# Kernel tuning notes

Measured on AMD Instinct MI355X. Metric: run time of the kernel, lower is better.

Reference implementation:

```python
import jax, jax.numpy as jnp
import numpy as np

N = 50000      # nodes
E = 1600000    # edges (avg degree 32)
D = 128        # feature dim (hardcoded by GATConv(128,128,1))
K = 3          # propagation order
NEG_SLOPE = 0.2  # DGL GATConv default leaky_relu slope


def setup_inputs() -> dict:
    key = jax.random.key(0)
    k1, k2, k3, k4, k5, k6, k7 = jax.random.split(key, 7)
    feats = jax.random.normal(k1, (N, D), dtype=jnp.float32)
    src = jax.random.randint(k2, (E,), 0, N, dtype=jnp.int32)
    dst = jax.random.randint(k3, (E,), 0, N, dtype=jnp.int32)
    W = jax.random.normal(k4, (D, D), dtype=jnp.float32) * 0.05
    attn_l = jax.random.normal(k5, (D,), dtype=jnp.float32) * 0.05
    attn_r = jax.random.normal(k6, (D,), dtype=jnp.float32) * 0.05
    bias = jax.random.normal(k7, (D,), dtype=jnp.float32) * 0.05
    return {"feats": feats, "W": W, "attn_l": attn_l, "attn_r": attn_r,
            "bias": bias, "src": src, "dst": dst}


def _grand_conv(feats, src, dst, order):
    seg = jax.ops.segment_sum
    ones = jnp.ones((src.shape[0],), feats.dtype)
    deg_in = jnp.maximum(seg(ones, dst, num_segments=N), 1.0)
    deg_out = jnp.maximum(seg(ones, src, num_segments=N), 1.0)
    norm1 = deg_in ** -0.5   # dst-side (in-degree) norm
    norm2 = deg_out ** -0.5  # src-side (out-degree) norm
    # rst = D_in^-1/2 A D_out^-1/2 feats  (one SpMM)
    nf = feats * norm2[:, None]
    rst = seg(nf[src], dst, num_segments=N) * norm1[:, None]
    # edge weight = norm1[src] * norm2[dst]  (fn.u_mul_v)
    w = (norm1[src] * norm2[dst])[:, None]  # [E,1]
    x = rst
    y = feats  # note: rst itself is NOT added (faithful to source)
    for _ in range(order):
        x = seg(x[src] * w, dst, num_segments=N)  # SpMM hop
        y = y + x
    return y / (order + 1)


def _gat(feat, W, attn_l, attn_r, bias, src, dst):
    seg = jax.ops.segment_sum
    h = feat @ W                      # [N,D]
    el = h @ attn_l                   # [N]
    er = h @ attn_r                   # [N]
    e = jax.nn.leaky_relu(el[src] + er[dst], NEG_SLOPE)  # [E]
    m = jax.ops.segment_max(e, dst, num_segments=N)      # stable edge-softmax
    a = jnp.exp(e - m[dst])
    s = seg(a, dst, num_segments=N)
    alpha = a / s[dst]
    out = seg(h[src] * alpha[:, None], dst, num_segments=N)
    return jax.nn.relu(out + bias)


def reference(feats, W, attn_l, attn_r, bias, src, dst):
    # drop_node with rate 0.0 is identity; S=1 so stacked mean is identity too.
    feat = _grand_conv(feats, src, dst, K)
    logits = _gat(feat, W, attn_l, attn_r, bias, src, dst)
    return jax.nn.log_softmax(logits, axis=-1)
```

## Files before the change

kernel.cpp:

```cpp
#include <hip/hip_runtime.h>
#include <hip/hip_bf16.h>
#include <math.h>

#define D 128
#define SB 512
#define GNUM 256
#define MAXW4 12512

typedef __attribute__((ext_vector_type(8))) short bf16x8;
typedef __attribute__((ext_vector_type(4))) float f32x4;
typedef __attribute__((ext_vector_type(2))) float fv2;

__device__ __forceinline__ bf16x8 pack8(const float* r) {
    union { bf16x8 v; __hip_bfloat162 h[4]; } u;
#pragma unroll
    for (int i = 0; i < 4; ++i)
        u.h[i] = __float22bfloat162_rn(make_float2(r[2 * i], r[2 * i + 1]));
    return u.v;
}

__device__ __forceinline__ uint2 packfp8x8(const float* r) {
    unsigned int w0 = 0, w1 = 0;
    w0 = __builtin_amdgcn_cvt_pk_fp8_f32(r[0], r[1], w0, false);
    w0 = __builtin_amdgcn_cvt_pk_fp8_f32(r[2], r[3], w0, true);
    w1 = __builtin_amdgcn_cvt_pk_fp8_f32(r[4], r[5], w1, false);
    w1 = __builtin_amdgcn_cvt_pk_fp8_f32(r[6], r[7], w1, true);
    return make_uint2(w0, w1);
}

__device__ __forceinline__ uint4 packfp8x16(const float* r) {
    uint4 o;
    unsigned int w;
    w = 0;
    w = __builtin_amdgcn_cvt_pk_fp8_f32(r[0], r[1], w, false);
    w = __builtin_amdgcn_cvt_pk_fp8_f32(r[2], r[3], w, true);
    o.x = w;
    w = 0;
    w = __builtin_amdgcn_cvt_pk_fp8_f32(r[4], r[5], w, false);
    w = __builtin_amdgcn_cvt_pk_fp8_f32(r[6], r[7], w, true);
    o.y = w;
    w = 0;
    w = __builtin_amdgcn_cvt_pk_fp8_f32(r[8], r[9], w, false);
    w = __builtin_amdgcn_cvt_pk_fp8_f32(r[10], r[11], w, true);
    o.z = w;
    w = 0;
    w = __builtin_amdgcn_cvt_pk_fp8_f32(r[12], r[13], w, false);
    w = __builtin_amdgcn_cvt_pk_fp8_f32(r[14], r[15], w, true);
    o.w = w;
    return o;
}

__device__ __forceinline__ void acc_fp8x16(uint4 v, fv2* a) {
    a[0] += __builtin_amdgcn_cvt_pk_f32_fp8(v.x, false);
    a[1] += __builtin_amdgcn_cvt_pk_f32_fp8(v.x, true);
    a[2] += __builtin_amdgcn_cvt_pk_f32_fp8(v.y, false);
    a[3] += __builtin_amdgcn_cvt_pk_f32_fp8(v.y, true);
    a[4] += __builtin_amdgcn_cvt_pk_f32_fp8(v.z, false);
    a[5] += __builtin_amdgcn_cvt_pk_f32_fp8(v.z, true);
    a[6] += __builtin_amdgcn_cvt_pk_f32_fp8(v.w, false);
    a[7] += __builtin_amdgcn_cvt_pk_f32_fp8(v.w, true);
}

__device__ __forceinline__ void acc_fp8x16w(uint4 v, float w, fv2* a) {
    fv2 wv = {w, w};
    a[0] += wv * __builtin_amdgcn_cvt_pk_f32_fp8(v.x, false);
    a[1] += wv * __builtin_amdgcn_cvt_pk_f32_fp8(v.x, true);
    a[2] += wv * __builtin_amdgcn_cvt_pk_f32_fp8(v.y, false);
    a[3] += wv * __builtin_amdgcn_cvt_pk_f32_fp8(v.y, true);
    a[4] += wv * __builtin_amdgcn_cvt_pk_f32_fp8(v.z, false);
    a[5] += wv * __builtin_amdgcn_cvt_pk_f32_fp8(v.z, true);
    a[6] += wv * __builtin_amdgcn_cvt_pk_f32_fp8(v.w, false);
    a[7] += wv * __builtin_amdgcn_cvt_pk_f32_fp8(v.w, true);
}

__device__ __forceinline__ float fast_exp2(float x) {
#if __has_builtin(__builtin_amdgcn_exp2f)
    return __builtin_amdgcn_exp2f(x);
#else
    return exp2f(x);
#endif
}

__global__ __launch_bounds__(256) void histo_both(const int* __restrict__ src,
                                                  const int* __restrict__ dst,
                                                  unsigned int* __restrict__ Hs,
                                                  unsigned int* __restrict__ Hd,
                                                  int E, int N) {
    __shared__ unsigned int h[2 * MAXW4];
    int words = (N + 3) >> 2;
    for (int i = threadIdx.x; i < 2 * words; i += 256) h[i] = 0;
    __syncthreads();
    int per = (E + GNUM - 1) / GNUM;
    int lo = blockIdx.x * per;
    int hi = min(E, lo + per);
    for (int e = lo + (int)threadIdx.x; e < hi; e += 256) {
        int s = src[e];
        int d = dst[e];
        atomicAdd(&h[s >> 2], 1u << ((s & 3) * 8));
        atomicAdd(&h[words + (d >> 2)], 1u << ((d & 3) * 8));
    }
    __syncthreads();
    unsigned int* hsrow = Hs + (size_t)blockIdx.x * words;
    unsigned int* hdrow = Hd + (size_t)blockIdx.x * words;
    for (int i = threadIdx.x; i < words; i += 256) {
        hsrow[i] = h[i];
        hdrow[i] = h[words + i];
    }
}

__global__ void col_sum8(const unsigned char* __restrict__ H, float* __restrict__ n2, int N) {
    int bin = blockIdx.x * blockDim.x + threadIdx.x;
    if (bin >= N) return;
    size_t stride = (size_t)(((N + 3) >> 2) * 4);
    unsigned int s = 0;
    for (int b = 0; b < GNUM; ++b) s += H[(size_t)b * stride + bin];
    n2[bin] = rsqrtf((float)max((int)s, 1));
}

__global__ void col_scan8(unsigned char* __restrict__ Hd, int* __restrict__ deg_in,
                          float* __restrict__ n1, int N) {
    int bin = blockIdx.x * blockDim.x + threadIdx.x;
    if (bin >= N) return;
    size_t stride = (size_t)(((N + 3) >> 2) * 4);
    unsigned int run = 0;
    for (int b = 0; b < GNUM; ++b) {
        size_t o = (size_t)b * stride + bin;
        unsigned int hv = Hd[o];
        Hd[o] = (unsigned char)run;
        run += hv;
    }
    deg_in[bin] = (int)run;
    n1[bin] = rsqrtf((float)max((int)run, 1));
}

__global__ void scan_blocks(const int* __restrict__ in, int* __restrict__ out,
                            int* __restrict__ sums, int n) {
    __shared__ int sh[SB];
    int gid = blockIdx.x * SB + threadIdx.x;
    int v = (gid < n) ? in[gid] : 0;
    sh[threadIdx.x] = v;
    __syncthreads();
    for (int off = 1; off < SB; off <<= 1) {
        int t = (threadIdx.x >= off) ? sh[threadIdx.x - off] : 0;
        __syncthreads();
        sh[threadIdx.x] += t;
        __syncthreads();
    }
    if (gid < n) out[gid] = sh[threadIdx.x] - v;
    if (threadIdx.x == SB - 1) sums[blockIdx.x] = sh[threadIdx.x];
}

__global__ void scan_sums(int* sums, int nb) {
    __shared__ int sh[SB];
    int v = (threadIdx.x < nb) ? sums[threadIdx.x] : 0;
    sh[threadIdx.x] = v;
    __syncthreads();
    for (int off = 1; off < SB; off <<= 1) {
        int t = (threadIdx.x >= off) ? sh[threadIdx.x - off] : 0;
        __syncthreads();
        sh[threadIdx.x] += t;
        __syncthreads();
    }
    if (threadIdx.x < nb) sums[threadIdx.x] = sh[threadIdx.x] - v;
}

__global__ void scan_add(int* out, const int* __restrict__ sums, int n, int E) {
    int gid = blockIdx.x * SB + threadIdx.x;
    if (gid < n) out[gid] += sums[blockIdx.x];
    if (blockIdx.x == 0 && threadIdx.x == 0) out[n] = E;
}

__global__ __launch_bounds__(256) void fill_part(const int* __restrict__ src,
                                                 const int* __restrict__ dst,
                                                 const int* __restrict__ rowp,
                                                 const unsigned char* __restrict__ base,
                                                 int* __restrict__ csr, int E, int N) {
    __shared__ unsigned int cur[MAXW4];
    int words = (N + 3) >> 2;
    for (int i = threadIdx.x; i < words; i += 256) cur[i] = 0;
    __syncthreads();
    size_t stride = (size_t)(words * 4);
    int per = (E + GNUM - 1) / GNUM;
    int lo = blockIdx.x * per;
    int hi = min(E, lo + per);
    const unsigned char* brow = base + (size_t)blockIdx.x * stride;
    for (int e = lo + (int)threadIdx.x; e < hi; e += 256) {
        int d = dst[e];
        unsigned int sh = (d & 3) * 8;
        unsigned int r = atomicAdd(&cur[d >> 2], 1u << sh);
        int rank = (int)((r >> sh) & 0xFFu);
        int pos = rowp[d] + (int)brow[d] + rank;
        csr[pos] = src[e];
    }
}

__global__ void convert_nf8(const float* __restrict__ feats, const float* __restrict__ n2,
                            unsigned int* __restrict__ nf8, int N) {
    int t = blockIdx.x * blockDim.x + threadIdx.x;
    int n = t >> 5, l = t & 31;
    if (n >= N) return;
    float w = n2[n];
    float4 f = *reinterpret_cast<const float4*>(feats + (size_t)n * D + l * 4);
    unsigned int w0 = 0;
    w0 = __builtin_amdgcn_cvt_pk_fp8_f32(f.x * w, f.y * w, w0, false);
    w0 = __builtin_amdgcn_cvt_pk_fp8_f32(f.z * w, f.w * w, w0, true);
    nf8[(size_t)n * 32 + l] = w0;
}

__global__ void convert_W(const float* __restrict__ W, ushort* __restrict__ Wb) {
    int tid = blockIdx.x * blockDim.x + threadIdx.x;
    if (tid >= 2048) return;
    int c = tid >> 8, t = (tid >> 6) & 3, lane = tid & 63;
    int col = c * 16 + (lane & 15);
    int k0 = t * 32 + ((lane >> 4) << 3);
    ushort* outp = Wb + (size_t)tid * 8;
    for (int j = 0; j < 8; ++j) {
        __hip_bfloat16 b = __float2bfloat16(W[(size_t)(k0 + j) * D + col]);
        outp[j] = *reinterpret_cast<ushort*>(&b);
    }
}

template <int MODE>
__global__ __launch_bounds__(256) void spmmw(const uint4* __restrict__ xs16,
                                             const ushort* __restrict__ ypin,
                                             const float* __restrict__ feats,
                                             const int* __restrict__ rowp,
                                             const int* __restrict__ csr,
                                             const float* __restrict__ n1,
                                             const float* __restrict__ n2,
                                             ushort* __restrict__ yp,
                                             uint4* __restrict__ outs16, int N) {
    int lane = threadIdx.x & 63;
    int g = lane >> 3, c = lane & 7;
    int wid = ((blockIdx.x * blockDim.x + threadIdx.x) >> 6) * 8 + g;
    if (wid >= N) return;
    int beg = rowp[wid], end = rowp[wid + 1];
    fv2 acc2[8] = {{0.f, 0.f}, {0.f, 0.f}, {0.f, 0.f}, {0.f, 0.f},
                   {0.f, 0.f}, {0.f, 0.f}, {0.f, 0.f}, {0.f, 0.f}};
    int base = beg;
    int cur_s = (beg < end) ? csr[beg + min(c, end - beg - 1)] : 0;
    while (base < end) {
        int nb = base + 8;
        int next_s = 0;
        if (nb < end) next_s = csr[nb + min(c, end - nb - 1)];
        int kn = min(8, end - base);
        uint4 v[8];
#pragma unroll
        for (int k = 0; k < 8; ++k) {
            int sk = __shfl(cur_s, k, 8);
            if (k < kn) v[k] = xs16[(size_t)sk * 8 + c];
        }
#pragma unroll
        for (int k = 0; k < 8; ++k)
            if (k < kn) acc_fp8x16(v[k], acc2);
        cur_s = next_s;
        base = nb;
    }
    float acc[16];
#pragma unroll
    for (int j = 0; j < 8; ++j) {
        acc[2 * j] = acc2[j][0];
        acc[2 * j + 1] = acc2[j][1];
    }
    if (MODE == 0) {
        float s1 = n1[wid];
        float sc = s1 * s1;
        float r[16];
#pragma unroll
        for (int i = 0; i < 16; ++i) r[i] = acc[i] * sc;
        outs16[(size_t)wid * 8 + c] = packfp8x16(r);
    } else if (MODE == 1 || MODE == 2) {
        float sp = n2[wid];
        float ss = sp * n1[wid];
        float xv[16], rs[16];
#pragma unroll
        for (int i = 0; i < 16; ++i) { xv[i] = acc[i] * sp; rs[i] = acc[i] * ss; }
        if (MODE == 2) {
            const bf16x8* pv = reinterpret_cast<const bf16x8*>(ypin + (size_t)wid * 128 + c * 16);
#pragma unroll
            for (int hb = 0; hb < 2; ++hb) {
                bf16x8 prev = pv[hb];
                const __hip_bfloat162* h2 = reinterpret_cast<const __hip_bfloat162*>(&prev);
#pragma unroll
                for (int i = 0; i < 4; ++i) {
                    float2 v2 = __bfloat1622float2(h2[i]);
                    xv[8 * hb + 2 * i] += v2.x;
                    xv[8 * hb + 2 * i + 1] += v2.y;
                }
            }
        }
        bf16x8* ov = reinterpret_cast<bf16x8*>(yp + (size_t)wid * 128 + c * 16);
        ov[0] = pack8(xv);
        ov[1] = pack8(xv + 8);
        outs16[(size_t)wid * 8 + c] = packfp8x16(rs);
    } else {
        float sp = n2[wid];
        float ft[16];
#pragma unroll
        for (int q4 = 0; q4 < 4; ++q4) {
            float4 f = *reinterpret_cast<const float4*>(feats + (size_t)wid * D + c * 16 + q4 * 4);
            ft[4 * q4] = f.x; ft[4 * q4 + 1] = f.y; ft[4 * q4 + 2] = f.z; ft[4 * q4 + 3] = f.w;
        }
        float r[16];
        const bf16x8* pv = reinterpret_cast<const bf16x8*>(ypin + (size_t)wid * 128 + c * 16);
#pragma unroll
        for (int hb = 0; hb < 2; ++hb) {
            bf16x8 prev = pv[hb];
            const __hip_bfloat162* h2 = reinterpret_cast<const __hip_bfloat162*>(&prev);
#pragma unroll
            for (int i = 0; i < 4; ++i) {
                float2 v2 = __bfloat1622float2(h2[i]);
                r[8 * hb + 2 * i]     = 0.25f * (ft[8 * hb + 2 * i] + v2.x + acc[8 * hb + 2 * i] * sp);
                r[8 * hb + 2 * i + 1] = 0.25f * (ft[8 * hb + 2 * i + 1] + v2.y + acc[8 * hb + 2 * i + 1] * sp);
            }
        }
        bf16x8* ov = reinterpret_cast<bf16x8*>(yp + (size_t)wid * 128 + c * 16);
        ov[0] = pack8(r);
        ov[1] = pack8(r + 8);
    }
}

__global__ __launch_bounds__(256) void gatw(const uint4* __restrict__ h16,
                                            const int* __restrict__ rowp,
                                            const int* __restrict__ csr,
                                            const float2* __restrict__ elsc,
                                            const float* __restrict__ er,
                                            const float* __restrict__ bias,
                                            float* __restrict__ out, int N) {
    int lane = threadIdx.x & 63;
    int g = lane >> 3, c = lane & 7;
    int wid = ((blockIdx.x * blockDim.x + threadIdx.x) >> 6) * 8 + g;
    if (wid >= N) return;
    int beg = rowp[wid], end = rowp[wid + 1];
    float ern = er[wid];
    float psum = 0.f;
    fv2 acc2[8] = {{0.f, 0.f}, {0.f, 0.f}, {0.f, 0.f}, {0.f, 0.f},
                   {0.f, 0.f}, {0.f, 0.f}, {0.f, 0.f}, {0.f, 0.f}};
    int base = beg;
    int cur_s = (beg < end) ? csr[beg + min(c, end - beg - 1)] : 0;
    while (base < end) {
        int nb = base + 8;
        int next_s = 0;
        if (nb < end) next_s = csr[nb + min(c, end - nb - 1)];
        int kn = min(8, end - base);
        float2 es = elsc[cur_s];
        float t = es.x + ern;
        t = fmaxf(t, 0.2f * t);
        float p = (c < kn) ? fast_exp2(t) : 0.f;
        psum += p;
        float wv = p * es.y;
        uint4 v[8];
#pragma unroll
        for (int k = 0; k < 8; ++k) {
            int sk = __shfl(cur_s, k, 8);
            if (k < kn) v[k] = h16[(size_t)sk * 8 + c];
        }
#pragma unroll
        for (int k = 0; k < 8; ++k)
            if (k < kn) {
                float wk = __shfl(wv, k, 8);
                acc_fp8x16w(v[k], wk, acc2);
            }
        cur_s = next_s;
        base = nb;
    }
    psum += __shfl_xor(psum, 1, 8);
    psum += __shfl_xor(psum, 2, 8);
    psum += __shfl_xor(psum, 4, 8);
    float inv = psum > 0.f ? 1.f / psum : 0.f;
    float zA[8], zB[8];
    float mx = -INFINITY;
#pragma unroll
    for (int j = 0; j < 8; ++j) {
        float2 b2 = *reinterpret_cast<const float2*>(bias + 16 * j + 2 * c);
        zA[j] = fmaxf(acc2[j >> 1][j & 1] * inv + b2.x, 0.f);
        zB[j] = fmaxf(acc2[(j + 8) >> 1][(j + 8) & 1] * inv + b2.y, 0.f);
        mx = fmaxf(mx, fmaxf(zA[j], zB[j]));
    }
    mx = fmaxf(mx, __shfl_xor(mx, 1, 8));
    mx = fmaxf(mx, __shfl_xor(mx, 2, 8));
    mx = fmaxf(mx, __shfl_xor(mx, 4, 8));
    float pz = 0.f;
#pragma unroll
    for (int j = 0; j < 8; ++j) pz += __expf(zA[j] - mx) + __expf(zB[j] - mx);
    pz += __shfl_xor(pz, 1, 8);
    pz += __shfl_xor(pz, 2, 8);
    pz += __shfl_xor(pz, 4, 8);
    float ls = logf(pz);
    float* op = out + (size_t)wid * D;
#pragma unroll
    for (int j = 0; j < 8; ++j) {
        float2 o2 = make_float2(zA[j] - mx - ls, zB[j] - mx - ls);
        *reinterpret_cast<float2*>(op + 16 * j + 2 * c) = o2;
    }
}

__global__ __launch_bounds__(256) void gemm_mfma(const ushort* __restrict__ ybf,
                                                 const ushort* __restrict__ Wb,
                                                 const float* __restrict__ attnl,
                                                 const float* __restrict__ attnr,
                                                 unsigned char* __restrict__ h8,
                                                 float2* __restrict__ elsc,
                                                 float* __restrict__ er, int N) {
    __shared__ ushort Ws[16384];
    {
        const float4* srcv = reinterpret_cast<const float4*>(Wb);
        float4* dstv = reinterpret_cast<float4*>(Ws);
        for (int i = threadIdx.x; i < 2048; i += 256) dstv[i] = srcv[i];
    }
    __syncthreads();
    int wave = threadIdx.x >> 6, lane = threadIdx.x & 63;
    int base = blockIdx.x * 64 + wave * 16;
    if (base >= N) return;
    int col16 = lane & 15, rgrp = lane >> 4;

    int arow = base + col16;
    const bf16x8* yrow = reinterpret_cast<const bf16x8*>(ybf + (size_t)arow * 128);
    bf16x8 afrag[4];
#pragma unroll
    for (int t = 0; t < 4; ++t) afrag[t] = yrow[t * 4 + rgrp];

    const bf16x8* WsV = reinterpret_cast<const bf16x8*>(Ws);
    f32x4 acc[8];
#pragma unroll
    for (int c = 0; c < 8; ++c) acc[c] = (f32x4){0.f, 0.f, 0.f, 0.f};
#pragma unroll
    for (int c = 0; c < 8; ++c) {
#pragma unroll
        for (int t = 0; t < 4; ++t) {
            bf16x8 b = WsV[(c * 4 + t) * 64 + lane];
            acc[c] = __builtin_amdgcn_mfma_f32_16x16x32_bf16(afrag[t], b, acc[c], 0, 0, 0);
        }
    }

    float pl[4] = {0.f, 0.f, 0.f, 0.f}, pr[4] = {0.f, 0.f, 0.f, 0.f};
#pragma unroll
    for (int c = 0; c < 8; ++c) {
        float alc = attnl[c * 16 + col16];
        float arc = attnr[c * 16 + col16];
#pragma unroll
        for (int r = 0; r < 4; ++r) {
            pl[r] += acc[c][r] * alc;
            pr[r] += acc[c][r] * arc;
        }
    }
#pragma unroll
    for (int r = 0; r < 4; ++r) {
#pragma unroll
        for (int off = 8; off; off >>= 1) {
            pl[r] += __shfl_xor(pl[r], off);
            pr[r] += __shfl_xor(pr[r], off);
        }
    }

    float rmax[4];
#pragma unroll
    for (int r = 0; r < 4; ++r) {
        float m = 0.f;
#pragma unroll
        for (int c = 0; c < 8; ++c) m = fmaxf(m, fabsf(acc[c][r]));
#pragma unroll
        for (int off = 1; off < 16; off <<= 1) m = fmaxf(m, __shfl_xor(m, off));
        rmax[r] = fmaxf(m, 1e-20f);
    }

#pragma unroll
    for (int r = 0; r < 4; ++r) {
        float iv = 448.f / rmax[r];
        float rr[8];
#pragma unroll
        for (int c = 0; c < 8; ++c) rr[c] = acc[c][r] * iv;
        uint2 pk = packfp8x8(rr);
        int row = base + rgrp * 4 + r;
        *reinterpret_cast<uint2*>(h8 + (size_t)row * 128 + col16 * 8) = pk;
    }

    const float LOG2E = 1.44269504088896340736f;
    if (col16 == 0) {
#pragma unroll
        for (int r = 0; r < 4; ++r) {
            int row = base + rgrp * 4 + r;
            elsc[row] = make_float2(pl[r] * LOG2E, rmax[r] * (1.f / 448.f));
            er[row] = pr[r] * LOG2E;
        }
    }
}

extern "C" void kernel_launch(void* const* d_in, const int* in_sizes, int n_in,
                              void* d_out, int out_size, void* d_ws, size_t ws_size,
                              hipStream_t stream) {
    const float* feats  = (const float*)d_in[0];
    const float* W      = (const float*)d_in[1];
    const float* attn_l = (const float*)d_in[2];
    const float* attn_r = (const float*)d_in[3];
    const float* bias   = (const float*)d_in[4];
    const int*   src    = (const int*)d_in[5];
    const int*   dst    = (const int*)d_in[6];
    int N = in_sizes[0] / D;
    int E = in_sizes[5];
    float* out = (float*)d_out;

    char* p = (char*)d_ws;
    auto alloc = [&](size_t bytes) {
        char* r = p;
        p += (bytes + 255) & ~size_t(255);
        return r;
    };
    int*    deg_in = (int*)alloc((size_t)N * 4);
    int*    rowp   = (int*)alloc(((size_t)N + 1) * 4);
    int*    bsums  = (int*)alloc((size_t)SB * 4);
    float*  n1     = (float*)alloc((size_t)N * 4);
    float*  n2     = (float*)alloc((size_t)N * 4);
    float*  er     = (float*)alloc((size_t)N * 4);
    float2* elsc   = (float2*)alloc((size_t)N * 8);
    int*    csr    = (int*)alloc((size_t)E * 4);
    ushort* Wb     = (ushort*)alloc((size_t)16384 * 2);
    ushort* bufY1  = (ushort*)alloc((size_t)N * 128 * 2);
    ushort* bufY   = (ushort*)alloc((size_t)N * 128 * 2);
    uint4*  t0     = (uint4*)alloc((size_t)N * 8 * 16);
    uint4*  t1     = (uint4*)alloc((size_t)N * 8 * 16);
    uint4*  t2     = (uint4*)alloc((size_t)N * 8 * 16);
    unsigned int* Hs = (unsigned int*)bufY1;
    unsigned int* Hd = (unsigned int*)bufY;

    const int tb = 256;
    histo_both<<<GNUM, tb, 0, stream>>>(src, dst, Hs, Hd, E, N);
    col_sum8<<<(N + tb - 1) / tb, tb, 0, stream>>>((const unsigned char*)Hs, n2, N);
    col_scan8<<<(N + tb - 1) / tb, tb, 0, stream>>>((unsigned char*)Hd, deg_in, n1, N);
    int nb = (N + SB - 1) / SB;
    scan_blocks<<<nb, SB, 0, stream>>>(deg_in, rowp, bsums, N);
    scan_sums<<<1, SB, 0, stream>>>(bsums, nb);
    scan_add<<<nb, SB, 0, stream>>>(rowp, bsums, N, E);
    fill_part<<<GNUM, tb, 0, stream>>>(src, dst, rowp, (const unsigned char*)Hd, csr, E, N);
    convert_W<<<8, tb, 0, stream>>>(W, Wb);
    convert_nf8<<<((size_t)N * 32 + tb - 1) / tb, tb, 0, stream>>>(feats, n2,
                                                                   (unsigned int*)t1, N);

    int wgrid8 = (N + 31) / 32;
    spmmw<0><<<wgrid8, 256, 0, stream>>>(t1, nullptr, nullptr, rowp, csr, n1, n2,
                                         nullptr, t0, N);
    spmmw<1><<<wgrid8, 256, 0, stream>>>(t0, nullptr, nullptr, rowp, csr, n1, n2,
                                         bufY1, t1, N);
    spmmw<2><<<wgrid8, 256, 0, stream>>>(t1, bufY1, nullptr, rowp, csr, n1, n2,
                                         bufY1, t2, N);
    spmmw<3><<<wgrid8, 256, 0, stream>>>(t2, bufY1, feats, rowp, csr, n1, n2,
                                         bufY, nullptr, N);

    gemm_mfma<<<(N + 63) / 64, 256, 0, stream>>>(bufY, Wb, attn_l, attn_r,
                                                 (unsigned char*)t0, elsc, er, N);
    gatw<<<wgrid8, 256, 0, stream>>>((const uint4*)t0, rowp, csr, elsc, er, bias, out, N);
}
```

Baseline: 263.2 us.

## Double-buffer neighbor row gathers in SpMM and GAT kernels with full/remainder split

Restructures the per-node neighbor loops in spmmw and gatw so that the next batch of 8 fp8 feature rows is loaded into a second register buffer while the current batch is accumulated. Full groups of 8 edges run without per-element bounds checks, and the partial tail is handled separately. Addresses are computed with 32-bit shift/or instead of size_t multiplies. This aims to hide gather latency, at the cost of doubled vector registers (vA/vB), which may reduce occupancy.

```diff
diff --git a/kernel.cpp b/kernel.cpp
--- a/kernel.cpp
+++ b/kernel.cpp
@@ -235,26 +235,63 @@
     int wid = ((blockIdx.x * blockDim.x + threadIdx.x) >> 6) * 8 + g;
     if (wid >= N) return;
     int beg = rowp[wid], end = rowp[wid + 1];
+    int cnt = end - beg;
+    int nfull = cnt >> 3;
+    int rem = cnt & 7;
+    const char* xb = (const char*)xs16;
+    unsigned coff = (unsigned)(c << 4);
+    const int* cp = csr + beg + c;
     fv2 acc2[8] = {{0.f, 0.f}, {0.f, 0.f}, {0.f, 0.f}, {0.f, 0.f},
                    {0.f, 0.f}, {0.f, 0.f}, {0.f, 0.f}, {0.f, 0.f}};
-    int base = beg;
-    int cur_s = (beg < end) ? csr[beg + min(c, end - beg - 1)] : 0;
-    while (base < end) {
-        int nb = base + 8;
-        int next_s = 0;
-        if (nb < end) next_s = csr[nb + min(c, end - nb - 1)];
-        int kn = min(8, end - base);
-        uint4 v[8];
+    uint4 vA[8], vB[8];
+    if (nfull > 0) {
+        int sN = 0;
+        int s0 = cp[0];
 #pragma unroll
         for (int k = 0; k < 8; ++k) {
-            int sk = __shfl(cur_s, k, 8);
-            if (k < kn) v[k] = xs16[(size_t)sk * 8 + c];
-        }
-#pragma unroll
-        for (int k = 0; k < 8; ++k)
-            if (k < kn) acc_fp8x16(v[k], acc2);
-        cur_s = next_s;
-        base = nb;
+            int sk = __shfl(s0, k, 8);
+            vA[k] = *(const uint4*)(xb + ((((unsigned)sk) << 7) | coff));
+        }
+        if (nfull > 1) sN = cp[8];
+        int j = 0;
+        while (true) {
+            if (j + 1 < nfull) {
+                int s = sN;
+                if (j + 2 < nfull) sN = cp[(j + 2) * 8];
+#pragma unroll
+                for (int k = 0; k < 8; ++k) {
+                    int sk = __shfl(s, k, 8);
+                    vB[k] = *(const uint4*)(xb + ((((unsigned)sk) << 7) | coff));
+                }
+            }
+#pragma unroll
+            for (int k = 0; k < 8; ++k) acc_fp8x16(vA[k], acc2);
+            if (++j >= nfull) break;
+            if (j + 1 < nfull) {
+                int s = sN;
+                if (j + 2 < nfull) sN = cp[(j + 2) * 8];
+#pragma unroll
+                for (int k = 0; k < 8; ++k) {
+                    int sk = __shfl(s, k, 8);
+                    vA[k] = *(const uint4*)(xb + ((((unsigned)sk) << 7) | coff));
+                }
+            }
+#pragma unroll
+            for (int k = 0; k < 8; ++k) acc_fp8x16(vB[k], acc2);
+            if (++j >= nfull) break;
+        }
+    }
+    if (rem) {
+        int b = beg + nfull * 8;
+        int s = csr[b + min(c, rem - 1)];
+#pragma unroll
+        for (int k = 0; k < 8; ++k) {
+            int sk = __shfl(s, k, 8);
+            if (k < rem) {
+                uint4 v = *(const uint4*)(xb + ((((unsigned)sk) << 7) | coff));
+                acc_fp8x16(v, acc2);
+            }
+        }
     }
     float acc[16];
 #pragma unroll
@@ -332,37 +369,96 @@
     int wid = ((blockIdx.x * blockDim.x + threadIdx.x) >> 6) * 8 + g;
     if (wid >= N) return;
     int beg = rowp[wid], end = rowp[wid + 1];
+    int cnt = end - beg;
+    int nfull = cnt >> 3;
+    int rem = cnt & 7;
+    const char* xb = (const char*)h16;
+    unsigned coff = (unsigned)(c << 4);
+    const int* cp = csr + beg + c;
     float ern = er[wid];
     float psum = 0.f;
     fv2 acc2[8] = {{0.f, 0.f}, {0.f, 0.f}, {0.f, 0.f}, {0.f, 0.f},
                    {0.f, 0.f}, {0.f, 0.f}, {0.f, 0.f}, {0.f, 0.f}};
-    int base = beg;
-    int cur_s = (beg < end) ? csr[beg + min(c, end - beg - 1)] : 0;
-    while (base < end) {
-        int nb = base + 8;
-        int next_s = 0;
-        if (nb < end) next_s = csr[nb + min(c, end - nb - 1)];
-        int kn = min(8, end - base);
-        float2 es = elsc[cur_s];
+    uint4 vA[8], vB[8];
+    float2 esA, esB;
+    if (nfull > 0) {
+        int sN = 0;
+        int s0 = cp[0];
+        esA = elsc[s0];
+#pragma unroll
+        for (int k = 0; k < 8; ++k) {
+            int sk = __shfl(s0, k, 8);
+            vA[k] = *(const uint4*)(xb + ((((unsigned)sk) << 7) | coff));
+        }
+        if (nfull > 1) sN = cp[8];
+        int j = 0;
+        while (true) {
+            if (j + 1 < nfull) {
+                int s = sN;
+                if (j + 2 < nfull) sN = cp[(j + 2) * 8];
+                esB = elsc[s];
+#pragma unroll
+                for (int k = 0; k < 8; ++k) {
+                    int sk = __shfl(s, k, 8);
+                    vB[k] = *(const uint4*)(xb + ((((unsigned)sk) << 7) | coff));
+                }
+            }
+            {
+                float t = esA.x + ern;
+                t = fmaxf(t, 0.2f * t);
+                float p = fast_exp2(t);
+                psum += p;
+                float wv = p * esA.y;
+                float wk[8];
+#pragma unroll
+                for (int k = 0; k < 8; ++k) wk[k] = __shfl(wv, k, 8);
+#pragma unroll
+                for (int k = 0; k < 8; ++k) acc_fp8x16w(vA[k], wk[k], acc2);
+            }
+            if (++j >= nfull) break;
+            if (j + 1 < nfull) {
+                int s = sN;
+                if (j + 2 < nfull) sN = cp[(j + 2) * 8];
+                esA = elsc[s];
+#pragma unroll
+                for (int k = 0; k < 8; ++k) {
+                    int sk = __shfl(s, k, 8);
+                    vA[k] = *(const uint4*)(xb + ((((unsigned)sk) << 7) | coff));
+                }
+            }
+            {
+                float t = esB.x + ern;
+                t = fmaxf(t, 0.2f * t);
+                float p = fast_exp2(t);
+                psum += p;
+                float wv = p * esB.y;
+                float wk[8];
+#pragma unroll
+                for (int k = 0; k < 8; ++k) wk[k] = __shfl(wv, k, 8);
+#pragma unroll
+                for (int k = 0; k < 8; ++k) acc_fp8x16w(vB[k], wk[k], acc2);
+            }
+            if (++j >= nfull) break;
+        }
+    }
+    if (rem) {
+        int b = beg + nfull * 8;
+        int s = csr[b + min(c, rem - 1)];
+        float2 es = elsc[s];
         float t = es.x + ern;
         t = fmaxf(t, 0.2f * t);
-        float p = (c < kn) ? fast_exp2(t) : 0.f;
+        float p = (c < rem) ? fast_exp2(t) : 0.f;
         psum += p;
         float wv = p * es.y;
-        uint4 v[8];
 #pragma unroll
         for (int k = 0; k < 8; ++k) {
-            int sk = __shfl(cur_s, k, 8);
-            if (k < kn) v[k] = h16[(size_t)sk * 8 + c];
-        }
-#pragma unroll
-        for (int k = 0; k < 8; ++k)
-            if (k < kn) {
+            int sk = __shfl(s, k, 8);
+            if (k < rem) {
+                uint4 v = *(const uint4*)(xb + ((((unsigned)sk) << 7) | coff));
                 float wk = __shfl(wv, k, 8);
-                acc_fp8x16w(v[k], wk, acc2);
-            }
-        cur_s = next_s;
-        base = nb;
+                acc_fp8x16w(v, wk, acc2);
+            }
+        }
     }
     psum += __shfl_xor(psum, 1, 8);
     psum += __shfl_xor(psum, 2, 8);
```

New measurement: 269.6 us. +2.5%, slower.

## Split fp8 SpMM feature tables into column halves processed by separate launches

Applied to the files above, without the earlier changes.

Stores the fp8 propagated features as two planar half-tables (64 columns each) and runs each SpMM hop as two launches, one per half. Each launch gathers 8-byte chunks from a 3.2MB table instead of 16-byte chunks from a 6.4MB table, so the gather working set fits better in cache. The cost is reading CSR indices and row pointers twice, running twice as many kernel launches, and issuing smaller gather transactions. The GAT kernel also gets unused index-math variables and shift-based addressing.

```diff
diff --git a/kernel.cpp b/kernel.cpp
--- a/kernel.cpp
+++ b/kernel.cpp
@@ -28,37 +28,11 @@
     return make_uint2(w0, w1);
 }
 
-__device__ __forceinline__ uint4 packfp8x16(const float* r) {
-    uint4 o;
-    unsigned int w;
-    w = 0;
-    w = __builtin_amdgcn_cvt_pk_fp8_f32(r[0], r[1], w, false);
-    w = __builtin_amdgcn_cvt_pk_fp8_f32(r[2], r[3], w, true);
-    o.x = w;
-    w = 0;
-    w = __builtin_amdgcn_cvt_pk_fp8_f32(r[4], r[5], w, false);
-    w = __builtin_amdgcn_cvt_pk_fp8_f32(r[6], r[7], w, true);
-    o.y = w;
-    w = 0;
-    w = __builtin_amdgcn_cvt_pk_fp8_f32(r[8], r[9], w, false);
-    w = __builtin_amdgcn_cvt_pk_fp8_f32(r[10], r[11], w, true);
-    o.z = w;
-    w = 0;
-    w = __builtin_amdgcn_cvt_pk_fp8_f32(r[12], r[13], w, false);
-    w = __builtin_amdgcn_cvt_pk_fp8_f32(r[14], r[15], w, true);
-    o.w = w;
-    return o;
-}
-
-__device__ __forceinline__ void acc_fp8x16(uint4 v, fv2* a) {
+__device__ __forceinline__ void acc_fp8x8(uint2 v, fv2* a) {
     a[0] += __builtin_amdgcn_cvt_pk_f32_fp8(v.x, false);
     a[1] += __builtin_amdgcn_cvt_pk_f32_fp8(v.x, true);
     a[2] += __builtin_amdgcn_cvt_pk_f32_fp8(v.y, false);
     a[3] += __builtin_amdgcn_cvt_pk_f32_fp8(v.y, true);
-    a[4] += __builtin_amdgcn_cvt_pk_f32_fp8(v.z, false);
-    a[5] += __builtin_amdgcn_cvt_pk_f32_fp8(v.z, true);
-    a[6] += __builtin_amdgcn_cvt_pk_f32_fp8(v.w, false);
-    a[7] += __builtin_amdgcn_cvt_pk_f32_fp8(v.w, true);
 }
 
 __device__ __forceinline__ void acc_fp8x16w(uint4 v, float w, fv2* a) {
@@ -204,7 +178,9 @@
     unsigned int w0 = 0;
     w0 = __builtin_amdgcn_cvt_pk_fp8_f32(f.x * w, f.y * w, w0, false);
     w0 = __builtin_amdgcn_cvt_pk_fp8_f32(f.z * w, f.w * w, w0, true);
-    nf8[(size_t)n * 32 + l] = w0;
+    int half = l >> 4;
+    int inner = l & 15;
+    nf8[(size_t)half * N * 16 + (size_t)n * 16 + inner] = w0;
 }
 
 __global__ void convert_W(const float* __restrict__ W, ushort* __restrict__ Wb) {
@@ -220,8 +196,8 @@
     }
 }
 
-template <int MODE>
-__global__ __launch_bounds__(256) void spmmw(const uint4* __restrict__ xs16,
+template <int MODE, int HALF>
+__global__ __launch_bounds__(256) void spmmh(const unsigned char* __restrict__ xs,
                                              const ushort* __restrict__ ypin,
                                              const float* __restrict__ feats,
                                              const int* __restrict__ rowp,
@@ -229,14 +205,15 @@
                                              const float* __restrict__ n1,
                                              const float* __restrict__ n2,
                                              ushort* __restrict__ yp,
-                                             uint4* __restrict__ outs16, int N) {
+                                             unsigned char* __restrict__ outs, int N) {
     int lane = threadIdx.x & 63;
     int g = lane >> 3, c = lane & 7;
     int wid = ((blockIdx.x * blockDim.x + threadIdx.x) >> 6) * 8 + g;
     if (wid >= N) return;
     int beg = rowp[wid], end = rowp[wid + 1];
-    fv2 acc2[8] = {{0.f, 0.f}, {0.f, 0.f}, {0.f, 0.f}, {0.f, 0.f},
-                   {0.f, 0.f}, {0.f, 0.f}, {0.f, 0.f}, {0.f, 0.f}};
+    const unsigned char* xb = xs + (size_t)HALF * N * 64;
+    unsigned coff = (unsigned)(c << 3);
+    fv2 acc2[4] = {{0.f, 0.f}, {0.f, 0.f}, {0.f, 0.f}, {0.f, 0.f}};
     int base = beg;
     int cur_s = (beg < end) ? csr[beg + min(c, end - beg - 1)] : 0;
     while (base < end) {
@@ -244,79 +221,68 @@
         int next_s = 0;
         if (nb < end) next_s = csr[nb + min(c, end - nb - 1)];
         int kn = min(8, end - base);
-        uint4 v[8];
+        uint2 v[8];
 #pragma unroll
         for (int k = 0; k < 8; ++k) {
             int sk = __shfl(cur_s, k, 8);
-            if (k < kn) v[k] = xs16[(size_t)sk * 8 + c];
+            if (k < kn) v[k] = *(const uint2*)(xb + ((((unsigned)sk) << 6) | coff));
         }
 #pragma unroll
         for (int k = 0; k < 8; ++k)
-            if (k < kn) acc_fp8x16(v[k], acc2);
+            if (k < kn) acc_fp8x8(v[k], acc2);
         cur_s = next_s;
         base = nb;
     }
-    float acc[16];
-#pragma unroll
-    for (int j = 0; j < 8; ++j) {
+    float acc[8];
+#pragma unroll
+    for (int j = 0; j < 4; ++j) {
         acc[2 * j] = acc2[j][0];
         acc[2 * j + 1] = acc2[j][1];
     }
     if (MODE == 0) {
         float s1 = n1[wid];
         float sc = s1 * s1;
-        float r[16];
-#pragma unroll
-        for (int i = 0; i < 16; ++i) r[i] = acc[i] * sc;
-        outs16[(size_t)wid * 8 + c] = packfp8x16(r);
+        float r[8];
+#pragma unroll
+        for (int i = 0; i < 8; ++i) r[i] = acc[i] * sc;
+        *reinterpret_cast<uint2*>(outs + (size_t)HALF * N * 64 + (size_t)wid * 64 + coff) =
+            packfp8x8(r);
     } else if (MODE == 1 || MODE == 2) {
         float sp = n2[wid];
         float ss = sp * n1[wid];
-        float xv[16], rs[16];
-#pragma unroll
-        for (int i = 0; i < 16; ++i) { xv[i] = acc[i] * sp; rs[i] = acc[i] * ss; }
+        float xv[8], rs[8];
+#pragma unroll
+        for (int i = 0; i < 8; ++i) { xv[i] = acc[i] * sp; rs[i] = acc[i] * ss; }
         if (MODE == 2) {
-            const bf16x8* pv = reinterpret_cast<const bf16x8*>(ypin + (size_t)wid * 128 + c * 16);
-#pragma unroll
-            for (int hb = 0; hb < 2; ++hb) {
-                bf16x8 prev = pv[hb];
-                const __hip_bfloat162* h2 = reinterpret_cast<const __hip_bfloat162*>(&prev);
-#pragma unroll
-                for (int i = 0; i < 4; ++i) {
-                    float2 v2 = __bfloat1622float2(h2[i]);
-                    xv[8 * hb + 2 * i] += v2.x;
-                    xv[8 * hb + 2 * i + 1] += v2.y;
-                }
+            bf16x8 prev = *reinterpret_cast<const bf16x8*>(
+                ypin + (size_t)wid * 128 + HALF * 64 + c * 8);
+            const __hip_bfloat162* h2 = reinterpret_cast<const __hip_bfloat162*>(&prev);
+#pragma unroll
+            for (int i = 0; i < 4; ++i) {
+                float2 v2 = __bfloat1622float2(h2[i]);
+                xv[2 * i] += v2.x;
+                xv[2 * i + 1] += v2.y;
             }
         }
-        bf16x8* ov = reinterpret_cast<bf16x8*>(yp + (size_t)wid * 128 + c * 16);
-        ov[0] = pack8(xv);
-        ov[1] = pack8(xv + 8);
-        outs16[(size_t)wid * 8 + c] = packfp8x16(rs);
+        *reinterpret_cast<bf16x8*>(yp + (size_t)wid * 128 + HALF * 64 + c * 8) = pack8(xv);
+        *reinterpret_cast<uint2*>(outs + (size_t)HALF * N * 64 + (size_t)wid * 64 + coff) =
+            packfp8x8(rs);
     } else {
         float sp = n2[wid];
-        float ft[16];
-#pragma unroll
-        for (int q4 = 0; q4 < 4; ++q4) {
-            float4 f = *reinterpret_cast<const float4*>(feats + (size_t)wid * D + c * 16 + q4 * 4);
-            ft[4 * q4] = f.x; ft[4 * q4 + 1] = f.y; ft[4 * q4 + 2] = f.z; ft[4 * q4 + 3] = f.w;
-        }
-        float r[16];
-        const bf16x8* pv = reinterpret_cast<const bf16x8*>(ypin + (size_t)wid * 128 + c * 16);
-#pragma unroll
-        for (int hb = 0; hb < 2; ++hb) {
-            bf16x8 prev = pv[hb];
-            const __hip_bfloat162* h2 = reinterpret_cast<const __hip_bfloat162*>(&prev);
-#pragma unroll
-            for (int i = 0; i < 4; ++i) {
-                float2 v2 = __bfloat1622float2(h2[i]);
-                r[8 * hb + 2 * i]     = 0.25f * (ft[8 * hb + 2 * i] + v2.x + acc[8 * hb + 2 * i] * sp);
-                r[8 * hb + 2 * i + 1] = 0.25f * (ft[8 * hb + 2 * i + 1] + v2.y + acc[8 * hb + 2 * i + 1] * sp);
-            }
-        }
-        bf16x8* ov = reinterpret_cast<bf16x8*>(yp + (size_t)wid * 128 + c * 16);
-        ov[0] = pack8(r);
-        ov[1] = pack8(r + 8);
+        float4 f0 = *reinterpret_cast<const float4*>(feats + (size_t)wid * D + HALF * 64 + c * 8);
+        float4 f1 = *reinterpret_cast<const float4*>(feats + (size_t)wid * D + HALF * 64 + c * 8 + 4);
+        float ft[8] = {f0.x, f0.y, f0.z, f0.w, f1.x, f1.y, f1.z, f1.w};
+        bf16x8 prev = *reinterpret_cast<const bf16x8*>(
+            ypin + (size_t)wid * 128 + HALF * 64 + c * 8);
+        const __hip_bfloat162* h2 = reinterpret_cast<const __hip_bfloat162*>(&prev);
+        float r[8];
+#pragma unroll
+        for (int i = 0; i < 4; ++i) {
+            float2 v2 = __bfloat1622float2(h2[i]);
+            r[2 * i]     = 0.25f * (ft[2 * i] + v2.x + acc[2 * i] * sp);
+            r[2 * i + 1] = 0.25f * (ft[2 * i + 1] + v2.y + acc[2 * i + 1] * sp);
+        }
+        *reinterpret_cast<bf16x8*>(yp + (size_t)wid * 128 + HALF * 64 + c * 8) = pack8(r);
     }
 }
 
@@ -332,6 +298,12 @@
     int wid = ((blockIdx.x * blockDim.x + threadIdx.x) >> 6) * 8 + g;
     if (wid >= N) return;
     int beg = rowp[wid], end = rowp[wid + 1];
+    int cnt = end - beg;
+    int nfull = cnt >> 3;
+    int rem = cnt & 7;
+    const char* xb = (const char*)h16;
+    unsigned coff = (unsigned)(c << 4);
+    const int* cp = csr + beg + c;
     float ern = er[wid];
     float psum = 0.f;
     fv2 acc2[8] = {{0.f, 0.f}, {0.f, 0.f}, {0.f, 0.f}, {0.f, 0.f},
@@ -353,7 +325,7 @@
 #pragma unroll
         for (int k = 0; k < 8; ++k) {
             int sk = __shfl(cur_s, k, 8);
-            if (k < kn) v[k] = h16[(size_t)sk * 8 + c];
+            if (k < kn) v[k] = *(const uint4*)(xb + ((((unsigned)sk) << 7) | coff));
         }
 #pragma unroll
         for (int k = 0; k < 8; ++k)
@@ -364,6 +336,7 @@
         cur_s = next_s;
         base = nb;
     }
+    (void)nfull; (void)rem; (void)cp;
     psum += __shfl_xor(psum, 1, 8);
     psum += __shfl_xor(psum, 2, 8);
     psum += __shfl_xor(psum, 4, 8);
@@ -517,9 +490,9 @@
     ushort* Wb     = (ushort*)alloc((size_t)16384 * 2);
     ushort* bufY1  = (ushort*)alloc((size_t)N * 128 * 2);
     ushort* bufY   = (ushort*)alloc((size_t)N * 128 * 2);
-    uint4*  t0     = (uint4*)alloc((size_t)N * 8 * 16);
-    uint4*  t1     = (uint4*)alloc((size_t)N * 8 * 16);
-    uint4*  t2     = (uint4*)alloc((size_t)N * 8 * 16);
+    unsigned char* t0 = (unsigned char*)alloc((size_t)N * 128);
+    unsigned char* t1 = (unsigned char*)alloc((size_t)N * 128);
+    unsigned char* t2 = (unsigned char*)alloc((size_t)N * 128);
     unsigned int* Hs = (unsigned int*)bufY1;
     unsigned int* Hd = (unsigned int*)bufY;
 
@@ -537,14 +510,22 @@
                                                                    (unsigned int*)t1, N);
 
     int wgrid8 = (N + 31) / 32;
-    spmmw<0><<<wgrid8, 256, 0, stream>>>(t1, nullptr, nullptr, rowp, csr, n1, n2,
-                                         nullptr, t0, N);
-    spmmw<1><<<wgrid8, 256, 0, stream>>>(t0, nullptr, nullptr, rowp, csr, n1, n2,
-                                         bufY1, t1, N);
-    spmmw<2><<<wgrid8, 256, 0, stream>>>(t1, bufY1, nullptr, rowp, csr, n1, n2,
-                                         bufY1, t2, N);
-    spmmw<3><<<wgrid8, 256, 0, stream>>>(t2, bufY1, feats, rowp, csr, n1, n2,
-                                         bufY, nullptr, N);
+    spmmh<0, 0><<<wgrid8, 256, 0, stream>>>(t1, nullptr, nullptr, rowp, csr, n1, n2,
+                                            nullptr, t0, N);
+    spmmh<0, 1><<<wgrid8, 256, 0, stream>>>(t1, nullptr, nullptr, rowp, csr, n1, n2,
+                                            nullptr, t0, N);
+    spmmh<1, 0><<<wgrid8, 256, 0, stream>>>(t0, nullptr, nullptr, rowp, csr, n1, n2,
+                                            bufY1, t1, N);
+    spmmh<1, 1><<<wgrid8, 256, 0, stream>>>(t0, nullptr, nullptr, rowp, csr, n1, n2,
+                                            bufY1, t1, N);
+    spmmh<2, 0><<<wgrid8, 256, 0, stream>>>(t1, bufY1, nullptr, rowp, csr, n1, n2,
+                                            bufY1, t2, N);
+    spmmh<2, 1><<<wgrid8, 256, 0, stream>>>(t1, bufY1, nullptr, rowp, csr, n1, n2,
+                                            bufY1, t2, N);
+    spmmh<3, 0><<<wgrid8, 256, 0, stream>>>(t2, bufY1, feats, rowp, csr, n1, n2,
+                                            bufY, nullptr, N);
+    spmmh<3, 1><<<wgrid8, 256, 0, stream>>>(t2, bufY1, feats, rowp, csr, n1, n2,
+                                            bufY, nullptr, N);
 
     gemm_mfma<<<(N + 63) / 64, 256, 0, stream>>>(bufY, Wb, attn_l, attn_r,
                                                  (unsigned char*)t0, elsc, er, N);
```

Result: slower. 297.3 us (+13.0%).

## Bucket nodes by in-degree and process them in sorted order for load balance

Applied to the files above, without the earlier changes.

Merges the two column-reduction kernels into one pass and has it bin nodes into 32 in-degree classes. A small scan plus a scatter kernel then build a node permutation grouped by degree, so each wavefront's eight 8-lane groups handle nodes of similar degree in the SpMM and GAT kernels. This is meant to cut divergence, where groups idle while one long row finishes. It costs two extra small launches and breaks the spatial locality of output rows. The GAT gather address math is also simplified to 32-bit shift/or.

```diff
diff --git a/kernel.cpp b/kernel.cpp
--- a/kernel.cpp
+++ b/kernel.cpp
@@ -85,7 +85,9 @@
                                                   const int* __restrict__ dst,
                                                   unsigned int* __restrict__ Hs,
                                                   unsigned int* __restrict__ Hd,
+                                                  int* __restrict__ bins32,
                                                   int E, int N) {
+    if (blockIdx.x == 0 && threadIdx.x < 32) bins32[threadIdx.x] = 0;
     __shared__ unsigned int h[2 * MAXW4];
     int words = (N + 3) >> 2;
     for (int i = threadIdx.x; i < 2 * words; i += 256) h[i] = 0;
@@ -108,29 +110,67 @@
     }
 }
 
-__global__ void col_sum8(const unsigned char* __restrict__ H, float* __restrict__ n2, int N) {
-    int bin = blockIdx.x * blockDim.x + threadIdx.x;
-    if (bin >= N) return;
-    size_t stride = (size_t)(((N + 3) >> 2) * 4);
-    unsigned int s = 0;
-    for (int b = 0; b < GNUM; ++b) s += H[(size_t)b * stride + bin];
-    n2[bin] = rsqrtf((float)max((int)s, 1));
-}
-
-__global__ void col_scan8(unsigned char* __restrict__ Hd, int* __restrict__ deg_in,
-                          float* __restrict__ n1, int N) {
-    int bin = blockIdx.x * blockDim.x + threadIdx.x;
-    if (bin >= N) return;
-    size_t stride = (size_t)(((N + 3) >> 2) * 4);
-    unsigned int run = 0;
-    for (int b = 0; b < GNUM; ++b) {
-        size_t o = (size_t)b * stride + bin;
-        unsigned int hv = Hd[o];
-        Hd[o] = (unsigned char)run;
-        run += hv;
-    }
-    deg_in[bin] = (int)run;
-    n1[bin] = rsqrtf((float)max((int)run, 1));
+__global__ __launch_bounds__(256) void col_both(const unsigned char* __restrict__ Hs,
+                                                unsigned char* __restrict__ Hd,
+                                                int* __restrict__ deg_in,
+                                                float* __restrict__ n1,
+                                                float* __restrict__ n2,
+                                                int* __restrict__ bins32,
+                                                int* __restrict__ blkbase, int N) {
+    __shared__ unsigned int lb[32];
+    if (threadIdx.x < 32) lb[threadIdx.x] = 0;
+    __syncthreads();
+    int bin = blockIdx.x * 256 + threadIdx.x;
+    if (bin < N) {
+        size_t stride = (size_t)(((N + 3) >> 2) * 4);
+        unsigned int s = 0, run = 0;
+        for (int b = 0; b < GNUM; ++b) {
+            size_t o = (size_t)b * stride + bin;
+            s += Hs[o];
+            unsigned int hv = Hd[o];
+            Hd[o] = (unsigned char)run;
+            run += hv;
+        }
+        n2[bin] = rsqrtf((float)max((int)s, 1));
+        deg_in[bin] = (int)run;
+        n1[bin] = rsqrtf((float)max((int)run, 1));
+        int cc = min(31, (int)((run + 7) >> 3));
+        atomicAdd(&lb[cc], 1u);
+    }
+    __syncthreads();
+    if (threadIdx.x < 32) {
+        unsigned int cnt = lb[threadIdx.x];
+        int base = 0;
+        if (cnt) base = atomicAdd(&bins32[threadIdx.x], (int)cnt);
+        blkbase[blockIdx.x * 32 + threadIdx.x] = base;
+    }
+}
+
+__global__ void scan32k(int* __restrict__ bins32) {
+    int t = threadIdx.x;
+    int orig = (t < 32) ? bins32[t] : 0;
+    int v = orig;
+    for (int off = 1; off < 32; off <<= 1) {
+        int u = __shfl_up(v, off, 32);
+        if ((t & 31) >= off) v += u;
+    }
+    if (t < 32) bins32[t] = v - orig;
+}
+
+__global__ __launch_bounds__(256) void scatter_perm(const int* __restrict__ deg_in,
+                                                    const int* __restrict__ bins32,
+                                                    const int* __restrict__ blkbase,
+                                                    int* __restrict__ perm, int N) {
+    __shared__ unsigned int lb[32];
+    if (threadIdx.x < 32) lb[threadIdx.x] = 0;
+    __syncthreads();
+    int node = blockIdx.x * 256 + threadIdx.x;
+    if (node < N) {
+        int cc = min(31, (deg_in[node] + 7) >> 3);
+        unsigned int r = atomicAdd(&lb[cc], 1u);
+        int pos = bins32[cc] + blkbase[blockIdx.x * 32 + cc] + (int)r;
+        perm[pos] = node;
+    }
 }
 
 __global__ void scan_blocks(const int* __restrict__ in, int* __restrict__ out,
@@ -226,14 +266,16 @@
                                              const float* __restrict__ feats,
                                              const int* __restrict__ rowp,
                                              const int* __restrict__ csr,
+                                             const int* __restrict__ perm,
                                              const float* __restrict__ n1,
                                              const float* __restrict__ n2,
                                              ushort* __restrict__ yp,
                                              uint4* __restrict__ outs16, int N) {
     int lane = threadIdx.x & 63;
     int g = lane >> 3, c = lane & 7;
-    int wid = ((blockIdx.x * blockDim.x + threadIdx.x) >> 6) * 8 + g;
-    if (wid >= N) return;
+    int widx = ((blockIdx.x * blockDim.x + threadIdx.x) >> 6) * 8 + g;
+    if (widx >= N) return;
+    int wid = perm[widx];
     int beg = rowp[wid], end = rowp[wid + 1];
     fv2 acc2[8] = {{0.f, 0.f}, {0.f, 0.f}, {0.f, 0.f}, {0.f, 0.f},
                    {0.f, 0.f}, {0.f, 0.f}, {0.f, 0.f}, {0.f, 0.f}};
@@ -323,15 +365,19 @@
 __global__ __launch_bounds__(256) void gatw(const uint4* __restrict__ h16,
                                             const int* __restrict__ rowp,
                                             const int* __restrict__ csr,
+                                            const int* __restrict__ perm,
                                             const float2* __restrict__ elsc,
                                             const float* __restrict__ er,
                                             const float* __restrict__ bias,
                                             float* __restrict__ out, int N) {
     int lane = threadIdx.x & 63;
     int g = lane >> 3, c = lane & 7;
-    int wid = ((blockIdx.x * blockDim.x + threadIdx.x) >> 6) * 8 + g;
-    if (wid >= N) return;
+    int widx = ((blockIdx.x * blockDim.x + threadIdx.x) >> 6) * 8 + g;
+    if (widx >= N) return;
+    int wid = perm[widx];
     int beg = rowp[wid], end = rowp[wid + 1];
+    const char* xb = (const char*)h16;
+    unsigned coff = (unsigned)(c << 4);
     float ern = er[wid];
     float psum = 0.f;
     fv2 acc2[8] = {{0.f, 0.f}, {0.f, 0.f}, {0.f, 0.f}, {0.f, 0.f},
@@ -353,7 +399,7 @@
 #pragma unroll
         for (int k = 0; k < 8; ++k) {
             int sk = __shfl(cur_s, k, 8);
-            if (k < kn) v[k] = h16[(size_t)sk * 8 + c];
+            if (k < kn) v[k] = *(const uint4*)(xb + ((((unsigned)sk) << 7) | coff));
         }
 #pragma unroll
         for (int k = 0; k < 8; ++k)
@@ -506,9 +552,13 @@
         p += (bytes + 255) & ~size_t(255);
         return r;
     };
+    int nblk = (N + 255) / 256;
     int*    deg_in = (int*)alloc((size_t)N * 4);
     int*    rowp   = (int*)alloc(((size_t)N + 1) * 4);
     int*    bsums  = (int*)alloc((size_t)SB * 4);
+    int*    perm   = (int*)alloc((size_t)N * 4);
+    int*    bins32 = (int*)alloc(32 * 4);
+    int*    blkbase= (int*)alloc((size_t)nblk * 32 * 4);
     float*  n1     = (float*)alloc((size_t)N * 4);
     float*  n2     = (float*)alloc((size_t)N * 4);
     float*  er     = (float*)alloc((size_t)N * 4);
@@ -524,9 +574,11 @@
     unsigned int* Hd = (unsigned int*)bufY;
 
     const int tb = 256;
-    histo_both<<<GNUM, tb, 0, stream>>>(src, dst, Hs, Hd, E, N);
-    col_sum8<<<(N + tb - 1) / tb, tb, 0, stream>>>((const unsigned char*)Hs, n2, N);
-    col_scan8<<<(N + tb - 1) / tb, tb, 0, stream>>>((unsigned char*)Hd, deg_in, n1, N);
+    histo_both<<<GNUM, tb, 0, stream>>>(src, dst, Hs, Hd, bins32, E, N);
+    col_both<<<nblk, tb, 0, stream>>>((const unsigned char*)Hs, (unsigned char*)Hd,
+                                      deg_in, n1, n2, bins32, blkbase, N);
+    scan32k<<<1, 64, 0, stream>>>(bins32);
+    scatter_perm<<<nblk, tb, 0, stream>>>(deg_in, bins32, blkbase, perm, N);
     int nb = (N + SB - 1) / SB;
     scan_blocks<<<nb, SB, 0, stream>>>(deg_in, rowp, bsums, N);
     scan_sums<<<1, SB, 0, stream>>>(bsums, nb);
@@ -537,16 +589,17 @@
                                                                    (unsigned int*)t1, N);
 
     int wgrid8 = (N + 31) / 32;
-    spmmw<0><<<wgrid8, 256, 0, stream>>>(t1, nullptr, nullptr, rowp, csr, n1, n2,
+    spmmw<0><<<wgrid8, 256, 0, stream>>>(t1, nullptr, nullptr, rowp, csr, perm, n1, n2,
                                          nullptr, t0, N);
-    spmmw<1><<<wgrid8, 256, 0, stream>>>(t0, nullptr, nullptr, rowp, csr, n1, n2,
+    spmmw<1><<<wgrid8, 256, 0, stream>>>(t0, nullptr, nullptr, rowp, csr, perm, n1, n2,
                                          bufY1, t1, N);
-    spmmw<2><<<wgrid8, 256, 0, stream>>>(t1, bufY1, nullptr, rowp, csr, n1, n2,
+    spmmw<2><<<wgrid8, 256, 0, stream>>>(t1, bufY1, nullptr, rowp, csr, perm, n1, n2,
                                          bufY1, t2, N);
-    spmmw<3><<<wgrid8, 256, 0, stream>>>(t2, bufY1, feats, rowp, csr, n1, n2,
+    spmmw<3><<<wgrid8, 256, 0, stream>>>(t2, bufY1, feats, rowp, csr, perm, n1, n2,
                                          bufY, nullptr, N);
 
     gemm_mfma<<<(N + 63) / 64, 256, 0, stream>>>(bufY, Wb, attn_l, attn_r,
                                                  (unsigned char*)t0, elsc, er, N);
-    gatw<<<wgrid8, 256, 0, stream>>>((const uint4*)t0, rowp, csr, elsc, er, bias, out, N);
-}
+    gatw<<<wgrid8, 256, 0, stream>>>((const uint4*)t0, rowp, csr, perm, elsc, er, bias,
+                                     out, N);
+}
```

Result: no change. 258.7 us (-1.7%).
